# Kernel tuning notes

Hardware: AMD Instinct MI355X
Metric: run time of the kernel (lower is better)

Reference implementation:

```python
import jax, jax.numpy as jnp
import numpy as np

N = 50000      # nodes
E = 800000     # edges (avg degree 16)
IN = 256       # in_dim
HID = 128      # hid_dim
OUT = 1        # out_dim (binary logits for BCEWithLogitsLoss)


def _glorot(key, fan_in, fan_out):
    s = float(np.sqrt(6.0 / (fan_in + fan_out)))
    return jax.random.uniform(key, (fan_in, fan_out), jnp.float32, -s, s)


def setup_inputs() -> dict:
    key = jax.random.key(0)
    ks = jax.random.split(key, 8)
    x = jax.random.normal(ks[0], (N, IN), jnp.float32)
    edge_index = jax.random.randint(ks[1], (2, E), 0, N, dtype=jnp.int64)
    edge_weight = jax.random.uniform(ks[2], (E,), jnp.float32)  # variant-infer sigmoid weights in (0,1)
    return {
        "x": x,
        "edge_index": edge_index,
        "edge_weight": edge_weight,
        "W1": _glorot(ks[3], IN, HID),
        "b1": jnp.zeros((HID,), jnp.float32),
        "W2": _glorot(ks[4], HID, HID),
        "b2": jnp.zeros((HID,), jnp.float32),
        "Wc": _glorot(ks[5], HID, OUT),
        "bc": jnp.zeros((OUT,), jnp.float32),
    }


def _gcn_conv(x, W, b, src, dst, ew):
    # GCNConv with edge_weight: add self-loops (weight 1.0), symmetric normalization.
    h = x @ W  # [N, F_out]
    deg = jax.ops.segment_sum(ew, dst, num_segments=N) + 1.0  # self-loop weight
    dinv = jax.lax.rsqrt(deg)  # deg >= 1 due to self-loops
    norm = dinv[src] * ew * dinv[dst]  # [E]
    agg = jax.ops.segment_sum(h[src] * norm[:, None], dst, num_segments=N)
    # self-loop contribution: norm_ii = dinv_i * 1.0 * dinv_i
    return agg + h * (dinv * dinv)[:, None] + b


def reference(x, edge_index, edge_weight, W1, b1, W2, b2, Wc, bc):
    src, dst = edge_index[0], edge_index[1]
    # ConstructModel gcn branch: layer_num-1 = 2 stacked GCNConv, no activation in between
    h = _gcn_conv(x, W1, b1, src, dst, edge_weight)
    h = _gcn_conv(h, W2, b2, src, dst, edge_weight)
    # classifier head
    return h @ Wc + bc  # [N, OUT] logits
```

## Files before the change

kernel.cpp:

```cpp
#include <hip/hip_runtime.h>


static constexpr int NN   = 50000;
static constexpr int NE   = 800000;
static constexpr int IND  = 256;
static constexpr int HD   = 128;
static constexpr int NNP  = 50048;

static constexpr int NBUK = 782;
static constexpr int BCAP = 1536;
static constexpr int BIN_BLOCKS  = 128;
static constexpr int EPB         = NE / BIN_BLOCKS;
static constexpr int GEMV_BLOCKS = 3125;


__global__ __launch_bounds__(256) void prep_kernel(
        const float* __restrict__ W1, const float* __restrict__ b1,
        const float* __restrict__ W2, const float* __restrict__ b2,
        const float* __restrict__ Wc, const float* __restrict__ bc,
        float* __restrict__ w1c, float* __restrict__ consts,
        int* __restrict__ gcur) {
    __shared__ float s_w2c[HD];
    const int t = threadIdx.x;
    for (int i = t; i < NBUK; i += 256) gcur[i] = 0;
    if (t < HD) {
        float s = 0.f;
        for (int j = 0; j < HD; j++) s += W2[t * HD + j] * Wc[j];
        s_w2c[t] = s;
    }
    __syncthreads();
    {
        float s = 0.f;
        for (int k = 0; k < HD; k++) s += W1[t * HD + k] * s_w2c[k];
        w1c[t] = s;
    }
    if (t == 0) {
        float c1 = 0.f, c2 = 0.f;
        for (int k = 0; k < HD; k++) c1 += b1[k] * s_w2c[k];
        for (int j = 0; j < HD; j++) c2 += b2[j] * Wc[j];
        consts[0] = c1;
        consts[1] = c2 + bc[0];
    }
}


__global__ __launch_bounds__(256) void gemv_bin(
        const float* __restrict__ x, const float* __restrict__ w1c,
        float* __restrict__ z0,
        const int* __restrict__ src, const int* __restrict__ dst,
        const float* __restrict__ ew,
        int* __restrict__ gcur, uint2* __restrict__ bins) {
    __shared__ int hist[NBUK];
    __shared__ int cur[NBUK];

    if (blockIdx.x < BIN_BLOCKS) {
        const int t    = threadIdx.x;
        const int base = blockIdx.x * EPB;
        for (int i = t; i < NBUK; i += 256) hist[i] = 0;
        __syncthreads();
        for (int off = t; off < EPB; off += 256)
            atomicAdd(&hist[dst[base + off] >> 6], 1);
        __syncthreads();
        for (int i = t; i < NBUK; i += 256) {
            const int h = hist[i];
            cur[i] = h ? atomicAdd(&gcur[i], h) : 0;
        }
        __syncthreads();
        for (int off = t; off < EPB; off += 256) {
            const int e = base + off;
            const int d = dst[e];
            const int b = d >> 6;
            const int p = atomicAdd(&cur[b], 1);
            if (p < BCAP)
                bins[(size_t)b * BCAP + p] =
                    make_uint2((uint)src[e] | (((uint)d & 63u) << 16),
                               __float_as_uint(ew[e]));
        }
    } else {
        const int wid  = threadIdx.x >> 6;
        const int lane = threadIdx.x & 63;
        const int n0   = (blockIdx.x - BIN_BLOCKS) * 16 + wid * 4;
        const float4 wv = ((const float4*)w1c)[lane];
        const float4 x0 = *((const float4*)(x + (size_t)(n0 + 0) * IND) + lane);
        const float4 x1 = *((const float4*)(x + (size_t)(n0 + 1) * IND) + lane);
        const float4 x2 = *((const float4*)(x + (size_t)(n0 + 2) * IND) + lane);
        const float4 x3 = *((const float4*)(x + (size_t)(n0 + 3) * IND) + lane);
        float p0 = x0.x * wv.x + x0.y * wv.y + x0.z * wv.z + x0.w * wv.w;
        float p1 = x1.x * wv.x + x1.y * wv.y + x1.z * wv.z + x1.w * wv.w;
        float p2 = x2.x * wv.x + x2.y * wv.y + x2.z * wv.z + x2.w * wv.w;
        float p3 = x3.x * wv.x + x3.y * wv.y + x3.z * wv.z + x3.w * wv.w;
#pragma unroll
        for (int off = 32; off; off >>= 1) {
            p0 += __shfl_down(p0, off);
            p1 += __shfl_down(p1, off);
            p2 += __shfl_down(p2, off);
            p3 += __shfl_down(p3, off);
        }
        if (lane == 0) {
            z0[n0 + 0] = p0;
            z0[n0 + 1] = p1;
            z0[n0 + 2] = p2;
            z0[n0 + 3] = p3;
        }
    }
}


__global__ __launch_bounds__(256) void bindeg_kernel(
        const int* __restrict__ gcur, const uint2* __restrict__ bins,
        const float* __restrict__ z0, float2* __restrict__ dz0) {
    __shared__ float acc[64];
    const int b = blockIdx.x, t = threadIdx.x;
    if (t < 64) acc[t] = 0.f;
    __syncthreads();
    const int cnt = min(gcur[b], BCAP);
    for (int r = t; r < cnt; r += 256) {
        const uint2 q = bins[(size_t)b * BCAP + r];
        atomicAdd(&acc[(q.x >> 16) & 63u], __uint_as_float(q.y));
    }
    __syncthreads();
    if (t < 64) {
        const int n = b * 64 + t;
        if (n < NN) dz0[n] = make_float2(rsqrtf(acc[t] + 1.0f), z0[n]);
    }
}


template<bool LAST>
__global__ __launch_bounds__(256) void prop_kernel(
        const int* __restrict__ gcur, const uint2* __restrict__ bins,
        const float2* __restrict__ dzin, const float* __restrict__ consts,
        int cidx, float2* __restrict__ dzout, float* __restrict__ fout) {
    __shared__ float acc[64];
    const int b = blockIdx.x, t = threadIdx.x;
    if (t < 64) acc[t] = 0.f;
    __syncthreads();
    const int cnt = min(gcur[b], BCAP);
    for (int r = t; r < cnt; r += 256) {
        const uint2 q = bins[(size_t)b * BCAP + r];
        const float2 sz = dzin[q.x & 0xFFFFu];
        atomicAdd(&acc[(q.x >> 16) & 63u], __uint_as_float(q.y) * sz.x * sz.y);
    }
    __syncthreads();
    if (t < 64) {
        const int n = b * 64 + t;
        if (n < NN) {
            const float2 me = dzin[n];
            const float v = acc[t] * me.x + me.y * me.x * me.x + consts[cidx];
            if (LAST) fout[n] = v;
            else      dzout[n] = make_float2(me.x, v);
        }
    }
}


extern "C" void kernel_launch(void* const* d_in, const int* in_sizes, int n_in,
                              void* d_out, int out_size, void* d_ws, size_t ws_size,
                              hipStream_t stream) {
    const float* x   = (const float*)d_in[0];
    const int*   ei  = (const int*)d_in[1];
    const float* ew  = (const float*)d_in[2];
    const float* W1  = (const float*)d_in[3];
    const float* b1  = (const float*)d_in[4];
    const float* W2  = (const float*)d_in[5];
    const float* b2  = (const float*)d_in[6];
    const float* Wc  = (const float*)d_in[7];
    const float* bc  = (const float*)d_in[8];
    const int* src = ei;
    const int* dst = ei + NE;
    float* out = (float*)d_out;

    uint2*  bins   = (uint2*)d_ws;
    float2* dz0    = (float2*)(bins + (size_t)NBUK * BCAP);
    float2* dz1    = dz0 + NNP;
    float*  z0     = (float*)(dz1 + NNP);
    float*  w1c    = z0 + NNP;
    float*  consts = w1c + 256;
    int*    gcur   = (int*)(consts + 64);

    prep_kernel<<<1, 256, 0, stream>>>(W1, b1, W2, b2, Wc, bc, w1c, consts, gcur);

    gemv_bin<<<BIN_BLOCKS + GEMV_BLOCKS, 256, 0, stream>>>(
        x, w1c, z0, src, dst, ew, gcur, bins);

    bindeg_kernel<<<NBUK, 256, 0, stream>>>(gcur, bins, z0, dz0);

    prop_kernel<false><<<NBUK, 256, 0, stream>>>(gcur, bins, dz0, consts, 0, dz1, nullptr);
    prop_kernel<true><<<NBUK, 256, 0, stream>>>(gcur, bins, dz1, consts, 1, nullptr, out);
}
```

Before: 71.03 us.

## Widen dst buckets to 256 nodes and keep binned edges in registers

Each destination bucket now covers 256 nodes instead of 64, so there are 196 buckets with capacity 5120 each. The degree and propagation kernels use one thread per node with a 256-entry shared accumulator. The binning phase now uses twice as many blocks and reads src, dst and weight once into registers, reusing them for both the histogram and the scatter passes instead of reloading. The aim is to cut redundant global reads and per-bucket overhead. The risk is that only 196 blocks run the latency-bound gather kernels, which may underfill the GPU, and each block now serializes roughly four times as many edges.

Measured after the change: 59.39 us. -16.4%, faster.

```diff
diff --git a/kernel.cpp b/kernel.cpp
--- a/kernel.cpp
+++ b/kernel.cpp
@@ -7,10 +7,11 @@
 static constexpr int HD   = 128;
 static constexpr int NNP  = 50048;
 
-static constexpr int NBUK = 782;
-static constexpr int BCAP = 1536;
-static constexpr int BIN_BLOCKS  = 128;
+static constexpr int NBUK = 196;
+static constexpr int BCAP = 5120;
+static constexpr int BIN_BLOCKS  = 256;
 static constexpr int EPB         = NE / BIN_BLOCKS;
+static constexpr int SLOTS       = (EPB + 255) / 256;
 static constexpr int GEMV_BLOCKS = 3125;
 
 
@@ -22,7 +23,7 @@
         int* __restrict__ gcur) {
     __shared__ float s_w2c[HD];
     const int t = threadIdx.x;
-    for (int i = t; i < NBUK; i += 256) gcur[i] = 0;
+    if (t < NBUK) gcur[t] = 0;
     if (t < HD) {
         float s = 0.f;
         for (int j = 0; j < HD; j++) s += W2[t * HD + j] * Wc[j];
@@ -56,25 +57,39 @@
     if (blockIdx.x < BIN_BLOCKS) {
         const int t    = threadIdx.x;
         const int base = blockIdx.x * EPB;
-        for (int i = t; i < NBUK; i += 256) hist[i] = 0;
+        uint  key[SLOTS];
+        float wv[SLOTS];
+        if (t < NBUK) hist[t] = 0;
         __syncthreads();
-        for (int off = t; off < EPB; off += 256)
-            atomicAdd(&hist[dst[base + off] >> 6], 1);
+#pragma unroll
+        for (int k = 0; k < SLOTS; k++) {
+            const int off = k * 256 + t;
+            if (off < EPB) {
+                const int e = base + off;
+                const int d = dst[e];
+                const int b = d >> 8;
+                key[k] = (uint)src[e] | (((uint)d & 255u) << 16) | ((uint)b << 24);
+                wv[k]  = ew[e];
+                atomicAdd(&hist[b], 1);
+            } else {
+                key[k] = 0xFFFFFFFFu;
+            }
+        }
         __syncthreads();
-        for (int i = t; i < NBUK; i += 256) {
-            const int h = hist[i];
-            cur[i] = h ? atomicAdd(&gcur[i], h) : 0;
+        if (t < NBUK) {
+            const int h = hist[t];
+            cur[t] = h ? atomicAdd(&gcur[t], h) : 0;
         }
         __syncthreads();
-        for (int off = t; off < EPB; off += 256) {
-            const int e = base + off;
-            const int d = dst[e];
-            const int b = d >> 6;
-            const int p = atomicAdd(&cur[b], 1);
-            if (p < BCAP)
-                bins[(size_t)b * BCAP + p] =
-                    make_uint2((uint)src[e] | (((uint)d & 63u) << 16),
-                               __float_as_uint(ew[e]));
+#pragma unroll
+        for (int k = 0; k < SLOTS; k++) {
+            if (key[k] != 0xFFFFFFFFu) {
+                const int b = key[k] >> 24;
+                const int p = atomicAdd(&cur[b], 1);
+                if (p < BCAP)
+                    bins[(size_t)b * BCAP + p] =
+                        make_uint2(key[k] & 0xFFFFFFu, __float_as_uint(wv[k]));
+            }
         }
     } else {
         const int wid  = threadIdx.x >> 6;
@@ -109,20 +124,18 @@
 __global__ __launch_bounds__(256) void bindeg_kernel(
         const int* __restrict__ gcur, const uint2* __restrict__ bins,
         const float* __restrict__ z0, float2* __restrict__ dz0) {
-    __shared__ float acc[64];
+    __shared__ float acc[256];
     const int b = blockIdx.x, t = threadIdx.x;
-    if (t < 64) acc[t] = 0.f;
+    acc[t] = 0.f;
     __syncthreads();
     const int cnt = min(gcur[b], BCAP);
     for (int r = t; r < cnt; r += 256) {
         const uint2 q = bins[(size_t)b * BCAP + r];
-        atomicAdd(&acc[(q.x >> 16) & 63u], __uint_as_float(q.y));
-    }
-    __syncthreads();
-    if (t < 64) {
-        const int n = b * 64 + t;
-        if (n < NN) dz0[n] = make_float2(rsqrtf(acc[t] + 1.0f), z0[n]);
-    }
+        atomicAdd(&acc[(q.x >> 16) & 255u], __uint_as_float(q.y));
+    }
+    __syncthreads();
+    const int n = b * 256 + t;
+    if (n < NN) dz0[n] = make_float2(rsqrtf(acc[t] + 1.0f), z0[n]);
 }
 
 
@@ -131,25 +144,23 @@
         const int* __restrict__ gcur, const uint2* __restrict__ bins,
         const float2* __restrict__ dzin, const float* __restrict__ consts,
         int cidx, float2* __restrict__ dzout, float* __restrict__ fout) {
-    __shared__ float acc[64];
+    __shared__ float acc[256];
     const int b = blockIdx.x, t = threadIdx.x;
-    if (t < 64) acc[t] = 0.f;
+    acc[t] = 0.f;
     __syncthreads();
     const int cnt = min(gcur[b], BCAP);
     for (int r = t; r < cnt; r += 256) {
         const uint2 q = bins[(size_t)b * BCAP + r];
         const float2 sz = dzin[q.x & 0xFFFFu];
-        atomicAdd(&acc[(q.x >> 16) & 63u], __uint_as_float(q.y) * sz.x * sz.y);
-    }
-    __syncthreads();
-    if (t < 64) {
-        const int n = b * 64 + t;
-        if (n < NN) {
-            const float2 me = dzin[n];
-            const float v = acc[t] * me.x + me.y * me.x * me.x + consts[cidx];
-            if (LAST) fout[n] = v;
-            else      dzout[n] = make_float2(me.x, v);
-        }
+        atomicAdd(&acc[(q.x >> 16) & 255u], __uint_as_float(q.y) * sz.x * sz.y);
+    }
+    __syncthreads();
+    const int n = b * 256 + t;
+    if (n < NN) {
+        const float2 me = dzin[n];
+        const float v = acc[t] * me.x + me.y * me.x * me.x + consts[cidx];
+        if (LAST) fout[n] = v;
+        else      dzout[n] = make_float2(me.x, v);
     }
 }
 
```
